# Optimization experiments

Measured on AMD Instinct MI355X. Metric: run time of the kernel, lower is better.

Reference implementation:

```python
import jax, jax.numpy as jnp
import numpy as np

B, W = 8192, 64
EMBED, NUM_OP = 32, 256


def _extract_features(inst, pc):
    # inst, pc: [B, W] int32 -> [B, W, 12] float32 (matches extract_features)
    f = [
        ((inst >> 28) & 15) / 15.0,
        (inst & 255) / 255.0,
        ((inst >> 16) & 255) / 255.0,
        (pc & 255) / 255.0,
        ((pc >> 8) & 255) / 255.0,
        (inst & 31) / 31.0,
        ((inst >> 5) & 31) / 31.0,
        ((inst >> 30) & 3) / 3.0,
        ((inst >> 26) & 3) / 3.0,
        ((inst >> 31) & 1) * 1.0,
        ((inst >> 10) & 4095) / 4095.0,
        jnp.zeros(inst.shape, jnp.float32),
    ]
    return jnp.stack([x.astype(jnp.float32) for x in f], axis=-1)


def setup_inputs() -> dict:
    key = jax.random.key(0)
    k1, k2, k3, k4 = jax.random.split(key, 4)
    instructions = jax.random.randint(k1, (B, W), 0, 2147483647, dtype=jnp.int32)
    pc = jax.random.randint(k2, (B,), 0, 65536, dtype=jnp.int32)
    opcode_table = jax.random.normal(k3, (NUM_OP, EMBED), dtype=jnp.float32)
    feat_W = jax.random.normal(k4, (12, EMBED), dtype=jnp.float32) * 0.3
    feat_b = jnp.zeros((EMBED,), jnp.float32)
    hazard_weights = jnp.array([5.0, 0.5, 3.0, 5.0, -2.0], jnp.float32)
    return {
        "instructions": instructions,
        "pc": pc,
        "opcode_table": opcode_table,
        "feat_W": feat_W,
        "feat_b": feat_b,
        "hazard_weights": hazard_weights,
    }


def reference(instructions, pc, opcode_table, feat_W, feat_b, hazard_weights):
    b, w = instructions.shape
    pcw = jnp.broadcast_to(pc[:, None], (b, w))

    # encode_instructions (computed as in the torch forward; unused in hybrid path)
    opcodes = (instructions >> 24) & 255
    feats = _extract_features(instructions, pcw)              # [B, W, 12]
    emb = opcode_table[opcodes] + jax.nn.relu(feats @ feat_W + feat_b)  # [B, W, E]
    del emb  # dead in hybrid path (use_hybrid=True default)

    # predict_dependencies_hybrid, fully vectorized over the i<j pairs
    rd = instructions & 31
    rn = (instructions >> 5) & 31
    rm = (instructions >> 16) & 31
    rd_i = rd[:, :, None]  # producer i
    raw = ((rd_i == rn[:, None, :]) | (rd_i == rm[:, None, :])) & (rd_i < 31)
    waw = (rd_i == rd[:, None, :]) & (rd_i < 31) & (rd[:, None, :] < 31)
    score = (hazard_weights[0] * raw.astype(jnp.float32)
             + hazard_weights[2] * waw.astype(jnp.float32)
             + hazard_weights[4])
    upper = jnp.triu(jnp.ones((w, w), jnp.float32), k=1)      # j > i only
    dep_matrix = jax.nn.sigmoid(score) * upper                # [B, W, W]

    # schedule_execution with executed_mask = 0:
    # readiness[:, i] = prod_{j<i} (1 - dep[:, j, i]); dep is 0 for j>=i
    readiness = jnp.prod(1.0 - dep_matrix, axis=1)            # [B, W]
    return dep_matrix, readiness
```

## Files before the change

### kernel.cpp

```cpp
#include <hip/hip_runtime.h>


constexpr int Bv = 8192;
constexpr int Wv = 64;

__global__ __launch_bounds__(256) void ooo_kernel(
    const int* __restrict__ inst,
    const float* __restrict__ hw,
    float* __restrict__ dep,
    float* __restrict__ ready)
{
    const int b    = (blockIdx.x * blockDim.x + threadIdx.x) >> 6;
    const int lane = threadIdx.x & 63;

    const float h0 = hw[0], h2 = hw[2], h4 = hw[4];
    const float v00 = 1.f / (1.f + __expf(-(h4)));
    const float v10 = 1.f / (1.f + __expf(-(h0 + h4)));
    const float v01 = 1.f / (1.f + __expf(-(h2 + h4)));
    const float v11 = 1.f / (1.f + __expf(-(h0 + h2 + h4)));

    const int v   = inst[(size_t)b * Wv + lane];
    const int rn  = (v >> 5)  & 31;
    const int rm  = (v >> 16) & 31;
    const int rd  = v & 31;
    const int rdv = (rd < 31) ? rd : 64;

    float prod = 1.f;
    float* const dep_col = dep + (size_t)b * Wv * Wv + lane;

#pragma unroll 8
    for (int i = 0; i < Wv; ++i) {
        int rdi = __builtin_amdgcn_readlane(rd, i);
        rdi = (rdi < 31) ? rdi : 99;
        const bool raw = (rdi == rn) | (rdi == rm);
        const bool waw = (rdi == rdv);
        float d = waw ? (raw ? v11 : v01) : (raw ? v10 : v00);
        d = (lane > i) ? d : 0.f;
        __builtin_nontemporal_store(d, dep_col + i * Wv);
        prod *= (1.f - d);
    }
    ready[(size_t)b * Wv + lane] = prod;
}

extern "C" void kernel_launch(void* const* d_in, const int* in_sizes, int n_in,
                              void* d_out, int out_size, void* d_ws, size_t ws_size,
                              hipStream_t stream) {
    const int*   instructions   = (const int*)d_in[0];
    const float* hazard_weights = (const float*)d_in[5];

    float* dep   = (float*)d_out;
    float* ready = dep + (size_t)Bv * Wv * Wv;

    ooo_kernel<<<(Bv * Wv) / 256, 256, 0, stream>>>(instructions, hazard_weights,
                                                    dep, ready);
}
```

Measured before the change: 151.6 us.

## Remap wave so each lane writes float4 of four columns across row groups

Each lane now owns four consecutive columns j and handles one of four interleaved row subsets, so the dep matrix is written with 16-byte float4 stores instead of scalar nontemporal stores. Per-column products are combined across the four row groups with xor shuffles before the readiness write. This aims to cut store instruction count and widen memory transactions. It drops the nontemporal hint and adds shuffles and register pressure.

```diff
diff --git a/kernel.cpp b/kernel.cpp
--- a/kernel.cpp
+++ b/kernel.cpp
@@ -19,27 +19,52 @@
     const float v01 = 1.f / (1.f + __expf(-(h2 + h4)));
     const float v11 = 1.f / (1.f + __expf(-(h0 + h2 + h4)));
 
-    const int v   = inst[(size_t)b * Wv + lane];
-    const int rn  = (v >> 5)  & 31;
-    const int rm  = (v >> 16) & 31;
-    const int rd  = v & 31;
-    const int rdv = (rd < 31) ? rd : 64;
+    const int v  = inst[(size_t)b * Wv + lane];
+    const int rd = v & 31;
 
-    float prod = 1.f;
-    float* const dep_col = dep + (size_t)b * Wv * Wv + lane;
+    const int j0 = (lane & 15) << 2;
+    int  rnj[4], rmj[4], rdj[4];
+    bool jv[4];
+#pragma unroll
+    for (int q = 0; q < 4; ++q) {
+        const int vj = __shfl(v, j0 + q, 64);
+        rnj[q] = (vj >> 5)  & 31;
+        rmj[q] = (vj >> 16) & 31;
+        rdj[q] = vj & 31;
+        jv[q]  = rdj[q] < 31;
+    }
 
-#pragma unroll 8
-    for (int i = 0; i < Wv; ++i) {
-        int rdi = __builtin_amdgcn_readlane(rd, i);
+    const int isub = lane >> 4;
+    float prod[4] = {1.f, 1.f, 1.f, 1.f};
+    float* const out_base = dep + (size_t)b * Wv * Wv + isub * Wv + j0;
+
+#pragma unroll
+    for (int s = 0; s < 16; ++s) {
+        const int  i   = (s << 2) + isub;
+        int rdi = __shfl(rd, i, 64);
         rdi = (rdi < 31) ? rdi : 99;
-        const bool raw = (rdi == rn) | (rdi == rm);
-        const bool waw = (rdi == rdv);
-        float d = waw ? (raw ? v11 : v01) : (raw ? v10 : v00);
-        d = (lane > i) ? d : 0.f;
-        __builtin_nontemporal_store(d, dep_col + i * Wv);
-        prod *= (1.f - d);
+        float o[4];
+#pragma unroll
+        for (int q = 0; q < 4; ++q) {
+            const bool raw = (rdi == rnj[q]) | (rdi == rmj[q]);
+            const bool waw = jv[q] & (rdi == rdj[q]);
+            float d = waw ? (raw ? v11 : v01) : (raw ? v10 : v00);
+            d = ((j0 + q) > i) ? d : 0.f;
+            o[q] = d;
+            prod[q] *= (1.f - d);
+        }
+        *(float4*)(out_base + (s << 2) * Wv) = make_float4(o[0], o[1], o[2], o[3]);
     }
-    ready[(size_t)b * Wv + lane] = prod;
+
+#pragma unroll
+    for (int q = 0; q < 4; ++q) {
+        prod[q] *= __shfl_xor(prod[q], 16, 64);
+        prod[q] *= __shfl_xor(prod[q], 32, 64);
+    }
+    if (isub == 0) {
+        *(float4*)(ready + (size_t)b * Wv + j0) =
+            make_float4(prod[0], prod[1], prod[2], prod[3]);
+    }
 }
 
 extern "C" void kernel_launch(void* const* d_in, const int* in_sizes, int n_in,
```

Result: faster. 148.2 us (-2.2%).
